# Performance work log

Measured on AMD Instinct MI355X. Metric: run time of the kernel, lower is better.

Reference implementation:

```python
import jax, jax.numpy as jnp
import numpy as np

# DYNARCLOSS hyperparameters (init parameters = [s, k1, k2, k3])
S = 64.0
K1 = 1.0
K2 = 0.1
K3 = 0.4


def setup_inputs() -> dict:
    key = jax.random.key(0)
    k_log, k_lab, k_w = jax.random.split(key, 3)
    B, C, D = 2048, 100000, 128
    # logits are cosine similarities, must lie strictly in [-1, 1] for arccos
    logits = (jax.random.uniform(k_log, (B, C), dtype=jnp.float32) * 2.0 - 1.0) * 0.999
    labels = jax.random.randint(k_lab, (B,), 0, C)  # all valid (!= -1)
    w = jax.random.normal(k_w, (C, D), dtype=jnp.float32)
    weight_norm = w / jnp.linalg.norm(w, axis=1, keepdims=True)  # row-normalized
    return {"logits": logits, "labels": labels, "weight_norm": weight_norm}


def _margin(labels, weight_norm):
    # weight[labels] @ weight.T -> cos angle between each sample's class weight
    # and every class weight; clamp, knock out the true class (-2), then the
    # row max is the cosine to the NEAREST OTHER class weight.
    valid = labels != -1
    lab = jnp.where(valid, labels, 0)
    w_labels = weight_norm[lab]                                   # [B, D]
    w_costheta = jnp.clip(w_labels @ weight_norm.T, -1.0, 1.0)    # [B, C]
    B = labels.shape[0]
    w_costheta = w_costheta.at[jnp.arange(B), lab].add(
        jnp.where(valid, -2.0, 0.0))
    costheta_wn_wyi = jnp.max(w_costheta, axis=1)                 # [B]
    theta = jnp.arccos(costheta_wn_wyi)
    smooth = 0.03 * K3 / (1.0 + jnp.power(jnp.abs(theta - K1) * 20.0, 1.1))
    return jax.nn.relu(theta - K1) * K2 + K3 + smooth             # [B]


def reference(logits, labels, weight_norm):
    valid = labels != -1
    lab = jnp.where(valid, labels, 0)
    B = labels.shape[0]
    rows = jnp.arange(B)

    theta = jnp.arccos(logits)                                    # [B, C]
    margin = _margin(labels, weight_norm)                         # [B]
    target_theta = theta[rows, lab]
    new_target = jnp.where(valid, target_theta + margin, target_theta)
    theta = theta.at[rows, lab].set(new_target)
    return jnp.cos(theta) * S
```

## Files before the change

kernel.cpp:

```cpp
#include <hip/hip_runtime.h>
#include <math.h>

#define Bsz    2048
#define Ccnt   100000
#define Dd     128
#define CT     128
#define NMBLK  782
#define NCHUNK (Bsz / 32)
#define MFIRST 800
#define SBLKS  2400
#define GRID_G (MFIRST + SBLKS)
#define N4     (Bsz * (Ccnt / 4))

typedef short  bf16x8  __attribute__((ext_vector_type(8)));
typedef float  f32x16  __attribute__((ext_vector_type(16)));
typedef float  f32x4   __attribute__((ext_vector_type(4)));

static __device__ __forceinline__ unsigned int enc_f32(float f) {
    unsigned int u = __float_as_uint(f);
    return (u & 0x80000000u) ? ~u : (u | 0x80000000u);
}
static __device__ __forceinline__ float dec_f32(unsigned int u) {
    unsigned int b = (u & 0x80000000u) ? (u & 0x7fffffffu) : ~u;
    return __uint_as_float(b);
}
static __device__ __forceinline__ unsigned short f2bf(float f) {
    unsigned int u = __float_as_uint(f);
    unsigned int r = ((u >> 16) & 1u) + 0x7fffu;
    return (unsigned short)((u + r) >> 16);
}

__global__ __launch_bounds__(256) void prep_kernel(
    const int* __restrict__ labels,
    const float* __restrict__ wnorm,
    bf16x8* __restrict__ qpk,
    unsigned int* __restrict__ maxbuf)
{
    int tid = blockIdx.x * 256 + threadIdx.x;
    if (tid < Bsz) maxbuf[tid] = 0u;
    int b   = tid >> 4;
    int c8  = (tid & 15) << 3;
    if (b >= Bsz) return;
    int lab = labels[b];
    if (lab < 0) lab = 0;
    const float* src = wnorm + (size_t)lab * Dd + c8;
    float4 u = *reinterpret_cast<const float4*>(src);
    float4 v = *reinterpret_cast<const float4*>(src + 4);
    unsigned short o[8] = { f2bf(u.x), f2bf(u.y), f2bf(u.z), f2bf(u.w),
                            f2bf(v.x), f2bf(v.y), f2bf(v.z), f2bf(v.w) };
    int p = b >> 5, t = c8 >> 4, l = ((c8 >> 3) & 1) * 32 + (b & 31);
    qpk[(size_t)(p * 8 + t) * 64 + l] = *reinterpret_cast<bf16x8*>(o);
}

template<bool EDGE>
__device__ __forceinline__ void margin_chunks(
    const int* __restrict__ labels,
    const bf16x8* __restrict__ qpk,
    const bf16x8 (&afr)[8], int base_c, int lane,
    unsigned int* smax)
{
    const int lm  = lane & 31;
    const int lim = Ccnt - base_c;

    for (int ch = 0; ch < NCHUNK; ++ch) {
        const int s = ch * 32 + lm;
        const bf16x8* qw = qpk + (size_t)ch * 512;
        bf16x8 b0 = qw[0 * 64 + lane], b1 = qw[1 * 64 + lane];
        bf16x8 b2 = qw[2 * 64 + lane], b3 = qw[3 * 64 + lane];
        bf16x8 b4 = qw[4 * 64 + lane], b5 = qw[5 * 64 + lane];
        bf16x8 b6 = qw[6 * 64 + lane], b7 = qw[7 * 64 + lane];

        f32x16 acc = {};
        acc = __builtin_amdgcn_mfma_f32_32x32x16_bf16(afr[0], b0, acc, 0, 0, 0);
        acc = __builtin_amdgcn_mfma_f32_32x32x16_bf16(afr[1], b1, acc, 0, 0, 0);
        acc = __builtin_amdgcn_mfma_f32_32x32x16_bf16(afr[2], b2, acc, 0, 0, 0);
        acc = __builtin_amdgcn_mfma_f32_32x32x16_bf16(afr[3], b3, acc, 0, 0, 0);
        acc = __builtin_amdgcn_mfma_f32_32x32x16_bf16(afr[4], b4, acc, 0, 0, 0);
        acc = __builtin_amdgcn_mfma_f32_32x32x16_bf16(afr[5], b5, acc, 0, 0, 0);
        acc = __builtin_amdgcn_mfma_f32_32x32x16_bf16(afr[6], b6, acc, 0, 0, 0);
        acc = __builtin_amdgcn_mfma_f32_32x32x16_bf16(afr[7], b7, acc, 0, 0, 0);

        const int rel = labels[s] - base_c;

        float mm0 = -3.0f, mm1 = -3.0f, mm2 = -3.0f, mm3 = -3.0f;
#pragma unroll
        for (int r = 0; r < 16; ++r) {
            const int row = (r & 3) + 8 * (r >> 2);
            float tv = acc[r];
            bool kill = (rel == row);
            if (EDGE) kill = kill || (row >= lim);
            tv = kill ? -3.0f : tv;
            if ((r & 3) == 0) mm0 = fmaxf(mm0, tv);
            if ((r & 3) == 1) mm1 = fmaxf(mm1, tv);
            if ((r & 3) == 2) mm2 = fmaxf(mm2, tv);
            if ((r & 3) == 3) mm3 = fmaxf(mm3, tv);
        }
        float m = fmaxf(fmaxf(mm0, mm1), fmaxf(mm2, mm3));
        m = fmaxf(m, __shfl_xor(m, 32));
        if (lane < 32) atomicMax(&smax[s], enc_f32(m));
    }
}

__device__ __forceinline__ void margin_body(
    int mb,
    const int* __restrict__ labels,
    const float* __restrict__ wnorm,
    const bf16x8* __restrict__ qpk,
    unsigned int* __restrict__ maxbuf)
{
    __shared__ unsigned int smax[Bsz];
    for (int i = threadIdx.x; i < Bsz; i += 256) smax[i] = 0u;
    __syncthreads();

    const int wave  = threadIdx.x >> 6;
    const int lane  = threadIdx.x & 63;
    const int h     = lane >> 5;
    const int lm    = lane & 31;
    const int cbase = mb * CT + wave * 32;
    const int cls   = cbase + lm;
    const bool cvalid = cls < Ccnt;

    bf16x8 afr[8];
    {
        const float* wr = wnorm + (size_t)(cvalid ? cls : 0) * Dd + h * 8;
#pragma unroll
        for (int t = 0; t < 8; ++t) {
            float4 u = *reinterpret_cast<const float4*>(wr + t * 16);
            float4 v = *reinterpret_cast<const float4*>(wr + t * 16 + 4);
            if (!cvalid) { u = make_float4(0,0,0,0); v = make_float4(0,0,0,0); }
            unsigned short o[8] = { f2bf(u.x), f2bf(u.y), f2bf(u.z), f2bf(u.w),
                                    f2bf(v.x), f2bf(v.y), f2bf(v.z), f2bf(v.w) };
            afr[t] = *reinterpret_cast<bf16x8*>(o);
        }
    }
    const int base_c = cbase + 4 * h;

    if (mb == NMBLK - 1)
        margin_chunks<true >(labels, qpk, afr, base_c, lane, smax);
    else
        margin_chunks<false>(labels, qpk, afr, base_c, lane, smax);

    __syncthreads();
    for (int i = threadIdx.x; i < Bsz; i += 256)
        atomicMax(&maxbuf[i], smax[i]);
}

__device__ __forceinline__ void scale_body(
    int sidx, const f32x4* __restrict__ in, f32x4* __restrict__ out)
{
    const int stride = SBLKS * 2048;
    for (int i = sidx * 2048 + (int)threadIdx.x; i < N4; i += stride) {
        f32x4 v0 = __builtin_nontemporal_load(in + i);
        f32x4 v1 = __builtin_nontemporal_load(in + i + 256);
        f32x4 v2 = __builtin_nontemporal_load(in + i + 512);
        f32x4 v3 = __builtin_nontemporal_load(in + i + 768);
        f32x4 v4 = __builtin_nontemporal_load(in + i + 1024);
        f32x4 v5 = __builtin_nontemporal_load(in + i + 1280);
        f32x4 v6 = __builtin_nontemporal_load(in + i + 1536);
        f32x4 v7 = __builtin_nontemporal_load(in + i + 1792);
        v0 *= 64.f; v1 *= 64.f; v2 *= 64.f; v3 *= 64.f;
        v4 *= 64.f; v5 *= 64.f; v6 *= 64.f; v7 *= 64.f;
        __builtin_nontemporal_store(v0, out + i);
        __builtin_nontemporal_store(v1, out + i + 256);
        __builtin_nontemporal_store(v2, out + i + 512);
        __builtin_nontemporal_store(v3, out + i + 768);
        __builtin_nontemporal_store(v4, out + i + 1024);
        __builtin_nontemporal_store(v5, out + i + 1280);
        __builtin_nontemporal_store(v6, out + i + 1536);
        __builtin_nontemporal_store(v7, out + i + 1792);
    }
}

__global__ __launch_bounds__(256, 4) void mega_kernel(
    const int* __restrict__ labels,
    const float* __restrict__ wnorm,
    const bf16x8* __restrict__ qpk,
    unsigned int* __restrict__ maxbuf,
    const f32x4* __restrict__ in,
    f32x4* __restrict__ out)
{
    const int bid = blockIdx.x;
    if (bid < MFIRST) {
        if (bid < NMBLK)
            margin_body(bid, labels, wnorm, qpk, maxbuf);
    } else {
        scale_body(bid - MFIRST, in, out);
    }
}

__global__ void fixup_kernel(const float* __restrict__ logits,
                             const int* __restrict__ labels,
                             const unsigned int* __restrict__ maxbuf,
                             float* __restrict__ out)
{
    int b = blockIdx.x * blockDim.x + threadIdx.x;
    if (b >= Bsz) return;
    int lab = labels[b];
    if (lab < 0) return;
    float mx = dec_f32(maxbuf[b]);
    mx = fminf(fmaxf(mx, -1.f), 1.f);
    float theta  = acosf(mx);
    float d      = theta - 1.0f;
    float smooth = 0.012f / powf(1.0f + fabsf(d) * 20.0f, 1.1f);
    float margin = fmaxf(d, 0.f) * 0.1f + 0.4f + smooth;
    size_t off = (size_t)b * Ccnt + lab;
    float x = logits[off];
    out[off] = cosf(acosf(x) + margin) * 64.0f;
}

extern "C" void kernel_launch(void* const* d_in, const int* in_sizes, int n_in,
                              void* d_out, int out_size, void* d_ws, size_t ws_size,
                              hipStream_t stream)
{
    const float* logits = (const float*)d_in[0];
    const int*   labels = (const int*)d_in[1];
    const float* wnorm  = (const float*)d_in[2];
    float* out = (float*)d_out;

    unsigned int* maxbuf = (unsigned int*)d_ws;
    bf16x8*       qpk    = (bf16x8*)((char*)d_ws + 8192);

    prep_kernel<<<(Bsz * (Dd / 8) + 255) / 256, 256, 0, stream>>>(
        labels, wnorm, qpk, maxbuf);

    mega_kernel<<<GRID_G, 256, 0, stream>>>(
        labels, wnorm, qpk, maxbuf,
        (const f32x4*)logits, (f32x4*)out);

    fixup_kernel<<<(Bsz + 255) / 256, 256, 0, stream>>>(
        logits, labels, maxbuf, out);
}
```

Measured before the change: 321.7 us.

## Fuse fixup into mega kernel via last-block counter and halve margin blocks

Removes the separate fixup kernel launch: each block increments a global counter, and the last block to finish computes the per-row margin and patches the target-class outputs. Margin blocks drop from 800 to 400, each handling up to two class tiles, which gives more of the grid to the streaming scale work. This saves a launch and its gap, but it serialises the fixup onto one block at the tail and may make the margin path a longer critical path.

```diff
diff --git a/kernel.cpp b/kernel.cpp
--- a/kernel.cpp
+++ b/kernel.cpp
@@ -7,7 +7,7 @@
 #define CT     128
 #define NMBLK  782
 #define NCHUNK (Bsz / 32)
-#define MFIRST 800
+#define MFIRST 400
 #define SBLKS  2400
 #define GRID_G (MFIRST + SBLKS)
 #define N4     (Bsz * (Ccnt / 4))
@@ -34,9 +34,11 @@
     const int* __restrict__ labels,
     const float* __restrict__ wnorm,
     bf16x8* __restrict__ qpk,
-    unsigned int* __restrict__ maxbuf)
+    unsigned int* __restrict__ maxbuf,
+    unsigned int* __restrict__ cnt)
 {
     int tid = blockIdx.x * 256 + threadIdx.x;
+    if (tid == 0) *cnt = 0u;
     if (tid < Bsz) maxbuf[tid] = 0u;
     int b   = tid >> 4;
     int c8  = (tid & 15) << 3;
@@ -106,9 +108,9 @@
     const int* __restrict__ labels,
     const float* __restrict__ wnorm,
     const bf16x8* __restrict__ qpk,
-    unsigned int* __restrict__ maxbuf)
-{
-    __shared__ unsigned int smax[Bsz];
+    unsigned int* __restrict__ maxbuf,
+    unsigned int* smax)
+{
     for (int i = threadIdx.x; i < Bsz; i += 256) smax[i] = 0u;
     __syncthreads();
 
@@ -143,6 +145,7 @@
     __syncthreads();
     for (int i = threadIdx.x; i < Bsz; i += 256)
         atomicMax(&maxbuf[i], smax[i]);
+    __syncthreads();
 }
 
 __device__ __forceinline__ void scale_body(
@@ -177,35 +180,44 @@
     const bf16x8* __restrict__ qpk,
     unsigned int* __restrict__ maxbuf,
     const f32x4* __restrict__ in,
-    f32x4* __restrict__ out)
-{
+    f32x4* __restrict__ out,
+    unsigned int* __restrict__ cnt,
+    const float* __restrict__ logits)
+{
+    __shared__ unsigned int smax[Bsz];
+    __shared__ bool s_last;
+
     const int bid = blockIdx.x;
     if (bid < MFIRST) {
-        if (bid < NMBLK)
-            margin_body(bid, labels, wnorm, qpk, maxbuf);
+        margin_body(bid, labels, wnorm, qpk, maxbuf, smax);
+        if (bid + MFIRST < NMBLK)
+            margin_body(bid + MFIRST, labels, wnorm, qpk, maxbuf, smax);
     } else {
         scale_body(bid - MFIRST, in, out);
     }
-}
-
-__global__ void fixup_kernel(const float* __restrict__ logits,
-                             const int* __restrict__ labels,
-                             const unsigned int* __restrict__ maxbuf,
-                             float* __restrict__ out)
-{
-    int b = blockIdx.x * blockDim.x + threadIdx.x;
-    if (b >= Bsz) return;
-    int lab = labels[b];
-    if (lab < 0) return;
-    float mx = dec_f32(maxbuf[b]);
-    mx = fminf(fmaxf(mx, -1.f), 1.f);
-    float theta  = acosf(mx);
-    float d      = theta - 1.0f;
-    float smooth = 0.012f / powf(1.0f + fabsf(d) * 20.0f, 1.1f);
-    float margin = fmaxf(d, 0.f) * 0.1f + 0.4f + smooth;
-    size_t off = (size_t)b * Ccnt + lab;
-    float x = logits[off];
-    out[off] = cosf(acosf(x) + margin) * 64.0f;
+
+    __syncthreads();
+    if (threadIdx.x == 0) {
+        __threadfence();
+        s_last = (atomicAdd(cnt, 1u) == GRID_G - 1);
+    }
+    __syncthreads();
+    if (s_last) {
+        __threadfence();
+        for (int b = threadIdx.x; b < Bsz; b += 256) {
+            int lab = labels[b];
+            if (lab < 0) continue;
+            float mx = dec_f32(maxbuf[b]);
+            mx = fminf(fmaxf(mx, -1.f), 1.f);
+            float theta  = acosf(mx);
+            float d      = theta - 1.0f;
+            float smooth = 0.012f / powf(1.0f + fabsf(d) * 20.0f, 1.1f);
+            float margin = fmaxf(d, 0.f) * 0.1f + 0.4f + smooth;
+            size_t off = (size_t)b * Ccnt + lab;
+            float x = logits[off];
+            reinterpret_cast<float*>(out)[off] = cosf(acosf(x) + margin) * 64.0f;
+        }
+    }
 }
 
 extern "C" void kernel_launch(void* const* d_in, const int* in_sizes, int n_in,
@@ -218,15 +230,13 @@
     float* out = (float*)d_out;
 
     unsigned int* maxbuf = (unsigned int*)d_ws;
-    bf16x8*       qpk    = (bf16x8*)((char*)d_ws + 8192);
+    unsigned int* cnt    = (unsigned int*)((char*)d_ws + 8192);
+    bf16x8*       qpk    = (bf16x8*)((char*)d_ws + 16384);
 
     prep_kernel<<<(Bsz * (Dd / 8) + 255) / 256, 256, 0, stream>>>(
-        labels, wnorm, qpk, maxbuf);
+        labels, wnorm, qpk, maxbuf, cnt);
 
     mega_kernel<<<GRID_G, 256, 0, stream>>>(
         labels, wnorm, qpk, maxbuf,
-        (const f32x4*)logits, (f32x4*)out);
-
-    fixup_kernel<<<(Bsz + 255) / 256, 256, 0, stream>>>(
-        logits, labels, maxbuf, out);
-}
+        (const f32x4*)logits, (f32x4*)out, cnt, logits);
+}
```

New measurement: 565.8 us. +75.9%, slower.
